# Performance work log

Hardware: AMD Instinct MI355X
Metric: run time of the kernel (lower is better)

Reference implementation:

```python
import jax, jax.numpy as jnp
import numpy as np

B, S, E, H = 8, 512, 1024, 16
Dh = E // H
MAX_LEN = 512


def setup_inputs() -> dict:
    key = jax.random.key(0)
    ks = jax.random.split(key, 16)
    std = 1.0 / np.sqrt(E)
    inp = {
        "query": jax.random.normal(ks[0], (B, S, E), jnp.float32),
        "key": jax.random.normal(ks[1], (B, S, E), jnp.float32),
        "value": jax.random.normal(ks[2], (B, S, E), jnp.float32),
        "Wq": jax.random.normal(ks[3], (E, E), jnp.float32) * std,
        "bq": jax.random.normal(ks[4], (E,), jnp.float32) * std,
        "Wk": jax.random.normal(ks[5], (E, E), jnp.float32) * std,
        "bk": jax.random.normal(ks[6], (E,), jnp.float32) * std,
        "Wv": jax.random.normal(ks[7], (E, E), jnp.float32) * std,
        "bv": jax.random.normal(ks[8], (E,), jnp.float32) * std,
        "Wo": jax.random.normal(ks[9], (E, E), jnp.float32) * std,
        "bo": jax.random.normal(ks[10], (E,), jnp.float32) * std,
        "pos": jax.random.normal(ks[11], (MAX_LEN, 1, E), jnp.float32),
    }
    return inp


def reference(query, key, value, Wq, bq, Wk, bk, Wv, bv, Wo, bo, pos):
    b, sq, e = query.shape
    s = min(sq, key.shape[1])  # target_seq_length (static)
    scale = np.sqrt(Dh).astype(np.float32)
    pe = pos[:s, 0, :][None]  # [1, s, E] broadcast over batch
    q = query[:, :s] @ Wq.T + bq + pe
    k = key[:, :s] @ Wk.T + bk + pe
    v = value[:, :s] @ Wv.T + bv + pe
    # [b, s, H, Dh]
    q = q.reshape(b, s, H, Dh)
    k = k.reshape(b, s, H, Dh)
    v = v.reshape(b, s, H, Dh)
    scores = jnp.einsum("bqhd,bkhd->bhqk", q, k) / scale
    attn = jax.nn.softmax(scores, axis=-1)
    wv = jnp.einsum("bhqk,bkhd->bqhd", attn, v).reshape(b, s, e)
    return wv @ Wo.T + bo
```

## Files before the change

kernel.cpp:

```cpp
#include <hip/hip_runtime.h>
#include <hip/hip_bf16.h>

typedef __attribute__((ext_vector_type(8))) short bfx8;
typedef __attribute__((ext_vector_type(4))) short bfx4;
typedef __attribute__((ext_vector_type(4))) float fx4;

static __device__ __forceinline__ short f2bf(float f) {
  union { float f; unsigned u; } v; v.f = f;
  unsigned r = v.u + 0x7fffu + ((v.u >> 16) & 1u);
  return (short)(r >> 16);
}

static __device__ __forceinline__ void gld16(const void* g, void* l) {
  __builtin_amdgcn_global_load_lds(
      (const __attribute__((address_space(1))) void*)g,
      (__attribute__((address_space(3))) void*)l, 16, 0, 0);
}

constexpr int Bz = 8, Sq = 512, Em = 1024, Hn = 16, Dh = 64;
constexpr int Mrows = Bz * Sq;
constexpr size_t NE = (size_t)Mrows * Em;
constexpr size_t WE = (size_t)Em * Em;

__global__ __launch_bounds__(256) void convert_kernel(
    const float* __restrict__ q, const float* __restrict__ k,
    const float* __restrict__ v,
    const float* __restrict__ Wq, const float* __restrict__ Wk,
    const float* __restrict__ Wv, const float* __restrict__ Wo,
    short* __restrict__ qx, short* __restrict__ kx, short* __restrict__ vx,
    short* __restrict__ wqb, short* __restrict__ wkb,
    short* __restrict__ wvb, short* __restrict__ wob)
{
  const size_t c = (size_t)blockIdx.x * 256 + threadIdx.x;
  constexpr size_t CI = NE / 8;
  constexpr size_t CW = WE / 8;
  const float* src; short* dst; size_t off;
  if (c < 3 * CI) {
    const int sgi = (int)(c / CI);
    src = sgi == 0 ? q : sgi == 1 ? k : v;
    dst = sgi == 0 ? qx : sgi == 1 ? kx : vx;
    off = (c - (size_t)sgi * CI) * 8;
  } else {
    const size_t w = c - 3 * CI;
    const int sgi = (int)(w / CW);
    src = sgi == 0 ? Wq : sgi == 1 ? Wk : sgi == 2 ? Wv : Wo;
    dst = sgi == 0 ? wqb : sgi == 1 ? wkb : sgi == 2 ? wvb : wob;
    off = (w - (size_t)sgi * CW) * 8;
  }
  fx4 a = *(const fx4*)(src + off);
  fx4 b = *(const fx4*)(src + off + 4);
  bfx8 o = { f2bf(a[0]), f2bf(a[1]), f2bf(a[2]), f2bf(a[3]),
             f2bf(b[0]), f2bf(b[1]), f2bf(b[2]), f2bf(b[3]) };
  *(bfx8*)(dst + off) = o;
}

constexpr int LDP = 136;

__global__ __launch_bounds__(256) void gemm_qkv_bf16(
    const short* __restrict__ qx, const short* __restrict__ kx,
    const short* __restrict__ vx,
    const short* __restrict__ Wqb, const short* __restrict__ Wkb,
    const short* __restrict__ Wvb,
    const float* __restrict__ bq, const float* __restrict__ bk,
    const float* __restrict__ bv,
    const float* __restrict__ pos,
    short* __restrict__ qb, short* __restrict__ kb, short* __restrict__ vb)
{
  __shared__ short SM[128 * LDP];
  short* As = SM;
  short* Bs = SM + 4096;

  const int z = blockIdx.z;
  const short* X = (z == 0) ? qx : (z == 1) ? kx : vx;
  const short* W = (z == 0) ? Wqb : (z == 1) ? Wkb : Wvb;
  const float* bias = (z == 0) ? bq : (z == 1) ? bk : bv;
  short* dst = (z == 0) ? qb : (z == 1) ? kb : vb;

  const int m0 = blockIdx.x * 128;
  const int n0 = blockIdx.y * 128;
  const int t = threadIdx.x, lane = t & 63, wave = t >> 6;
  const int wr = wave >> 1, wc = wave & 1;
  const int fr = lane & 15, fq = lane >> 4;

  const int r0 = t >> 2, o0 = (t & 3) * 8;
  const int r1 = r0 + 64;
  short* lA0 = As + wave * 512;
  short* lA1 = As + 2048 + wave * 512;
  short* lB0 = Bs + wave * 512;
  short* lB1 = Bs + 2048 + wave * 512;

  fx4 acc[4][4] = {};

  for (int k0 = 0; k0 < Em; k0 += 32) {
    gld16(W + (size_t)(n0 + r0) * Em + k0 + o0, lA0);
    gld16(W + (size_t)(n0 + r1) * Em + k0 + o0, lA1);
    gld16(X + (size_t)(m0 + r0) * Em + k0 + o0, lB0);
    gld16(X + (size_t)(m0 + r1) * Em + k0 + o0, lB1);
    __syncthreads();

    bfx8 af[4], bf[4];
#pragma unroll
    for (int u = 0; u < 4; ++u)
      af[u] = *(const bfx8*)&As[(wr * 64 + u * 16 + fr) * 32 + fq * 8];
#pragma unroll
    for (int v = 0; v < 4; ++v)
      bf[v] = *(const bfx8*)&Bs[(wc * 64 + v * 16 + fr) * 32 + fq * 8];
#pragma unroll
    for (int u = 0; u < 4; ++u)
#pragma unroll
      for (int v = 0; v < 4; ++v)
        acc[u][v] = __builtin_amdgcn_mfma_f32_16x16x32_bf16(af[u], bf[v], acc[u][v], 0, 0, 0);
    __syncthreads();
  }

  const int rr = t >> 4, jj = t & 15;
  const int b = m0 >> 9;
  if (z < 2) {
#pragma unroll
    for (int u = 0; u < 4; ++u) {
      const int nn = wr * 64 + u * 16 + fq * 4;
      const int nng = n0 + nn;
      const fx4 bb = *(const fx4*)&bias[nng];
#pragma unroll
      for (int v = 0; v < 4; ++v) {
        const int m = wc * 64 + v * 16 + fr;
        const int s = (m0 + m) & (Sq - 1);
        const fx4 pe = *(const fx4*)&pos[(size_t)s * Em + nng];
        const fx4 a = acc[u][v];
        bfx4 o = { f2bf(a[0] + bb[0] + pe[0]), f2bf(a[1] + bb[1] + pe[1]),
                   f2bf(a[2] + bb[2] + pe[2]), f2bf(a[3] + bb[3] + pe[3]) };
        *(bfx4*)&SM[m * LDP + nn] = o;
      }
    }
    __syncthreads();
#pragma unroll
    for (int it = 0; it < 8; ++it) {
      const int m = it * 16 + rr;
      const int s = (m0 + m) & (Sq - 1);
      bfx8 val = *(const bfx8*)&SM[m * LDP + jj * 8];
      const int nng = n0 + jj * 8;
      const int h = nng >> 6, d = nng & 63;
      *(bfx8*)&dst[(((size_t)b * Hn + h) * Sq + s) * Dh + d] = val;
    }
  } else {
#pragma unroll
    for (int u = 0; u < 4; ++u) {
      const int nnb = wr * 64 + u * 16 + fq * 4;
      const int nng = n0 + nnb;
      const fx4 bb = *(const fx4*)&bias[nng];
#pragma unroll
      for (int v = 0; v < 4; ++v) {
        const int m = wc * 64 + v * 16 + fr;
        const int s = (m0 + m) & (Sq - 1);
        const fx4 pe = *(const fx4*)&pos[(size_t)s * Em + nng];
        const fx4 a = acc[u][v];
#pragma unroll
        for (int i = 0; i < 4; ++i) {
          const int row = nnb + i;
          SM[row * LDP + (m ^ ((row & 12) << 2))] = f2bf(a[i] + bb[i] + pe[i]);
        }
      }
    }
    __syncthreads();
    const int s0 = m0 & (Sq - 1);
#pragma unroll
    for (int it = 0; it < 8; ++it) {
      const int row = it * 16 + rr;
      bfx8 val = *(const bfx8*)&SM[row * LDP + ((jj * 8) ^ ((row & 12) << 2))];
      const int nng = n0 + row;
      const int h = nng >> 6, d = nng & 63;
      *(bfx8*)&dst[(((size_t)b * Hn + h) * Dh + d) * Sq + s0 + jj * 8] = val;
    }
  }
}

__global__ __launch_bounds__(256) void gemm_out_bf16(
    const short* __restrict__ wv, const short* __restrict__ Wob,
    const float* __restrict__ bo, float* __restrict__ out)
{
  __shared__ short As[128 * 32];
  __shared__ short Bs[128 * 32];

  const int m0 = blockIdx.x * 128;
  const int n0 = blockIdx.y * 128;
  const int t = threadIdx.x, lane = t & 63, wave = t >> 6;
  const int wr = wave >> 1, wc = wave & 1;
  const int fr = lane & 15, fq = lane >> 4;

  const int r0 = t >> 2, o0 = (t & 3) * 8;
  const int r1 = r0 + 64;
  short* lA0 = As + wave * 512;
  short* lA1 = As + 2048 + wave * 512;
  short* lB0 = Bs + wave * 512;
  short* lB1 = Bs + 2048 + wave * 512;

  fx4 acc[4][4] = {};

  for (int k0 = 0; k0 < Em; k0 += 32) {
    gld16(Wob + (size_t)(n0 + r0) * Em + k0 + o0, lA0);
    gld16(Wob + (size_t)(n0 + r1) * Em + k0 + o0, lA1);
    gld16(wv + (size_t)(m0 + r0) * Em + k0 + o0, lB0);
    gld16(wv + (size_t)(m0 + r1) * Em + k0 + o0, lB1);
    __syncthreads();

    bfx8 af[4], bf[4];
#pragma unroll
    for (int u = 0; u < 4; ++u)
      af[u] = *(const bfx8*)&As[(wr * 64 + u * 16 + fr) * 32 + fq * 8];
#pragma unroll
    for (int v = 0; v < 4; ++v)
      bf[v] = *(const bfx8*)&Bs[(wc * 64 + v * 16 + fr) * 32 + fq * 8];
#pragma unroll
    for (int u = 0; u < 4; ++u)
#pragma unroll
      for (int v = 0; v < 4; ++v)
        acc[u][v] = __builtin_amdgcn_mfma_f32_16x16x32_bf16(af[u], bf[v], acc[u][v], 0, 0, 0);
    __syncthreads();
  }

#pragma unroll
  for (int u = 0; u < 4; ++u) {
    const int nn = n0 + wr * 64 + u * 16 + fq * 4;
    const fx4 bb = *(const fx4*)&bo[nn];
#pragma unroll
    for (int v = 0; v < 4; ++v) {
      const int m = m0 + wc * 64 + v * 16 + fr;
      fx4 val = acc[u][v];
      val[0] += bb[0]; val[1] += bb[1]; val[2] += bb[2]; val[3] += bb[3];
      *(fx4*)&out[(size_t)m * Em + nn] = val;
    }
  }
}

constexpr int KVB = 64, LDK = 72;

__global__ __launch_bounds__(256) void attn_kernel(
    const short* __restrict__ qb, const short* __restrict__ kb,
    const short* __restrict__ vb, short* __restrict__ wv)
{
  __shared__ short Ks[KVB * LDK];
  __shared__ short Vt[Dh * LDK];
  __shared__ short Ps[4][16 * LDK];

  const int bh = blockIdx.x;
  const int qt = blockIdx.y;
  const int t = threadIdx.x, lane = t & 63, wave = t >> 6;
  const int fr = lane & 15, fq = lane >> 4;

  const size_t base = (size_t)bh * Sq * Dh;
  const int q0 = qt * 64 + wave * 16;

  bfx8 qf[2];
  {
    const short* qp = qb + base + (size_t)(q0 + fr) * Dh;
    qf[0] = *(const bfx8*)(qp + fq * 8);
    qf[1] = *(const bfx8*)(qp + 32 + fq * 8);
  }

  float mrow[4] = { -1e30f, -1e30f, -1e30f, -1e30f };
  float lrow[4] = { 0.f, 0.f, 0.f, 0.f };
  fx4 oacc[4] = {};

  const int kr = t >> 2, kc = (t & 3) * 16;

  for (int kv0 = 0; kv0 < Sq; kv0 += KVB) {
    {
      const short* kp = kb + base + (size_t)(kv0 + kr) * Dh + kc;
      bfx8 u0 = *(const bfx8*)kp;
      bfx8 u1 = *(const bfx8*)(kp + 8);
      *(bfx8*)&Ks[kr * LDK + kc] = u0;
      *(bfx8*)&Ks[kr * LDK + kc + 8] = u1;
    }
    {
      const short* vp = vb + base + (size_t)kr * Sq + kv0 + kc;
      bfx8 u0 = *(const bfx8*)vp;
      bfx8 u1 = *(const bfx8*)(vp + 8);
      *(bfx8*)&Vt[kr * LDK + kc] = u0;
      *(bfx8*)&Vt[kr * LDK + kc + 8] = u1;
    }
    __syncthreads();

    fx4 sa[4] = {};
#pragma unroll
    for (int nf = 0; nf < 4; ++nf) {
#pragma unroll
      for (int ks = 0; ks < 2; ++ks) {
        bfx8 kf = *(const bfx8*)&Ks[(nf * 16 + fr) * LDK + ks * 32 + fq * 8];
        sa[nf] = __builtin_amdgcn_mfma_f32_16x16x32_bf16(qf[ks], kf, sa[nf], 0, 0, 0);
      }
    }

#pragma unroll
    for (int i = 0; i < 4; ++i) {
      float mx = fmaxf(fmaxf(sa[0][i], sa[1][i]), fmaxf(sa[2][i], sa[3][i]));
      mx = fmaxf(mx, __shfl_xor(mx, 1));
      mx = fmaxf(mx, __shfl_xor(mx, 2));
      mx = fmaxf(mx, __shfl_xor(mx, 4));
      mx = fmaxf(mx, __shfl_xor(mx, 8));
      mx *= 0.125f;
      const float mn = fmaxf(mrow[i], mx);
      const float alpha = __expf(mrow[i] - mn);
      mrow[i] = mn;
      float rs = 0.f;
#pragma unroll
      for (int nf = 0; nf < 4; ++nf) {
        const float p = __expf(sa[nf][i] * 0.125f - mn);
        rs += p;
        Ps[wave][(fq * 4 + i) * LDK + nf * 16 + fr] = f2bf(p);
      }
      rs += __shfl_xor(rs, 1);
      rs += __shfl_xor(rs, 2);
      rs += __shfl_xor(rs, 4);
      rs += __shfl_xor(rs, 8);
      lrow[i] = lrow[i] * alpha + rs;
#pragma unroll
      for (int df = 0; df < 4; ++df) oacc[df][i] *= alpha;
    }
    __syncthreads();

    bfx8 pf[2];
    pf[0] = *(const bfx8*)&Ps[wave][fr * LDK + fq * 8];
    pf[1] = *(const bfx8*)&Ps[wave][fr * LDK + 32 + fq * 8];
#pragma unroll
    for (int df = 0; df < 4; ++df) {
#pragma unroll
      for (int ks = 0; ks < 2; ++ks) {
        bfx8 vf = *(const bfx8*)&Vt[(df * 16 + fr) * LDK + ks * 32 + fq * 8];
        oacc[df] = __builtin_amdgcn_mfma_f32_16x16x32_bf16(pf[ks], vf, oacc[df], 0, 0, 0);
      }
    }
    __syncthreads();
  }

  const int b = bh >> 4, h = bh & 15;
#pragma unroll
  for (int df = 0; df < 4; ++df) {
    const int d = df * 16 + fr;
#pragma unroll
    for (int i = 0; i < 4; ++i) {
      const int qrow = q0 + fq * 4 + i;
      const float o = oacc[df][i] / lrow[i];
      wv[((size_t)b * Sq + qrow) * Em + h * Dh + d] = f2bf(o);
    }
  }
}

extern "C" void kernel_launch(void* const* d_in, const int* in_sizes, int n_in,
                              void* d_out, int out_size, void* d_ws, size_t ws_size,
                              hipStream_t stream) {
  (void)in_sizes; (void)n_in; (void)out_size; (void)ws_size;
  const float* query = (const float*)d_in[0];
  const float* key   = (const float*)d_in[1];
  const float* value = (const float*)d_in[2];
  const float* Wq = (const float*)d_in[3];
  const float* bq = (const float*)d_in[4];
  const float* Wk = (const float*)d_in[5];
  const float* bk = (const float*)d_in[6];
  const float* Wv = (const float*)d_in[7];
  const float* bv = (const float*)d_in[8];
  const float* Wo = (const float*)d_in[9];
  const float* bo = (const float*)d_in[10];
  const float* pos = (const float*)d_in[11];

  short* qx = (short*)d_ws;
  short* kx = qx + NE;
  short* vx = kx + NE;
  short* Wqb = vx + NE;
  short* Wkb = Wqb + WE;
  short* Wvb = Wkb + WE;
  short* Wob = Wvb + WE;
  short* qb = Wob + WE;
  short* wv = qx;
  short* kb = (short*)d_out;
  short* vb = kb + NE;

  convert_kernel<<<dim3(8192), 256, 0, stream>>>(
      query, key, value, Wq, Wk, Wv, Wo, qx, kx, vx, Wqb, Wkb, Wvb, Wob);
  gemm_qkv_bf16<<<dim3(Mrows / 128, Em / 128, 3), 256, 0, stream>>>(
      qx, kx, vx, Wqb, Wkb, Wvb, bq, bk, bv, pos, qb, kb, vb);
  attn_kernel<<<dim3(Bz * Hn, Sq / 64), 256, 0, stream>>>(qb, kb, vb, wv);
  gemm_out_bf16<<<dim3(Mrows / 128, Em / 128), 256, 0, stream>>>(
      wv, Wob, bo, (float*)d_out);
}
```

Measured before the change: 125.5 us.

## Double-buffer LDS tiles in QKV and output projection GEMMs

```diff
diff --git a/kernel.cpp b/kernel.cpp
--- a/kernel.cpp
+++ b/kernel.cpp
@@ -67,8 +67,6 @@
     short* __restrict__ qb, short* __restrict__ kb, short* __restrict__ vb)
 {
   __shared__ short SM[128 * LDP];
-  short* As = SM;
-  short* Bs = SM + 4096;
 
   const int z = blockIdx.z;
   const short* X = (z == 0) ? qx : (z == 1) ? kx : vx;
@@ -84,32 +82,47 @@
 
   const int r0 = t >> 2, o0 = (t & 3) * 8;
   const int r1 = r0 + 64;
-  short* lA0 = As + wave * 512;
-  short* lA1 = As + 2048 + wave * 512;
-  short* lB0 = Bs + wave * 512;
-  short* lB1 = Bs + 2048 + wave * 512;
+  const short* gW0 = W + (size_t)(n0 + r0) * Em + o0;
+  const short* gW1 = W + (size_t)(n0 + r1) * Em + o0;
+  const short* gX0 = X + (size_t)(m0 + r0) * Em + o0;
+  const short* gX1 = X + (size_t)(m0 + r1) * Em + o0;
 
   fx4 acc[4][4] = {};
 
-  for (int k0 = 0; k0 < Em; k0 += 32) {
-    gld16(W + (size_t)(n0 + r0) * Em + k0 + o0, lA0);
-    gld16(W + (size_t)(n0 + r1) * Em + k0 + o0, lA1);
-    gld16(X + (size_t)(m0 + r0) * Em + k0 + o0, lB0);
-    gld16(X + (size_t)(m0 + r1) * Em + k0 + o0, lB1);
-    __syncthreads();
-
+  auto stage = [&](int kk, short* Ab, short* Bb) {
+    gld16(gW0 + kk, Ab + wave * 512);
+    gld16(gW1 + kk, Ab + 2048 + wave * 512);
+    gld16(gX0 + kk, Bb + wave * 512);
+    gld16(gX1 + kk, Bb + 2048 + wave * 512);
+  };
+  auto compute = [&](const short* Asb, const short* Bsb) {
     bfx8 af[4], bf[4];
 #pragma unroll
     for (int u = 0; u < 4; ++u)
-      af[u] = *(const bfx8*)&As[(wr * 64 + u * 16 + fr) * 32 + fq * 8];
+      af[u] = *(const bfx8*)&Asb[(wr * 64 + u * 16 + fr) * 32 + fq * 8];
 #pragma unroll
     for (int v = 0; v < 4; ++v)
-      bf[v] = *(const bfx8*)&Bs[(wc * 64 + v * 16 + fr) * 32 + fq * 8];
+      bf[v] = *(const bfx8*)&Bsb[(wc * 64 + v * 16 + fr) * 32 + fq * 8];
 #pragma unroll
     for (int u = 0; u < 4; ++u)
 #pragma unroll
       for (int v = 0; v < 4; ++v)
         acc[u][v] = __builtin_amdgcn_mfma_f32_16x16x32_bf16(af[u], bf[v], acc[u][v], 0, 0, 0);
+  };
+
+  short* A0 = SM;
+  short* B0 = SM + 4096;
+  short* A1 = SM + 8192;
+  short* B1 = SM + 12288;
+
+  stage(0, A0, B0);
+  __syncthreads();
+  for (int k0 = 0; k0 < Em; k0 += 64) {
+    stage(k0 + 32, A1, B1);
+    compute(A0, B0);
+    __syncthreads();
+    if (k0 + 64 < Em) stage(k0 + 64, A0, B0);
+    compute(A1, B1);
     __syncthreads();
   }
 
@@ -178,8 +191,7 @@
     const short* __restrict__ wv, const short* __restrict__ Wob,
     const float* __restrict__ bo, float* __restrict__ out)
 {
-  __shared__ short As[128 * 32];
-  __shared__ short Bs[128 * 32];
+  __shared__ short SM[4 * 4096];
 
   const int m0 = blockIdx.x * 128;
   const int n0 = blockIdx.y * 128;
@@ -189,32 +201,47 @@
 
   const int r0 = t >> 2, o0 = (t & 3) * 8;
   const int r1 = r0 + 64;
-  short* lA0 = As + wave * 512;
-  short* lA1 = As + 2048 + wave * 512;
-  short* lB0 = Bs + wave * 512;
-  short* lB1 = Bs + 2048 + wave * 512;
+  const short* gW0 = Wob + (size_t)(n0 + r0) * Em + o0;
+  const short* gW1 = Wob + (size_t)(n0 + r1) * Em + o0;
+  const short* gX0 = wv + (size_t)(m0 + r0) * Em + o0;
+  const short* gX1 = wv + (size_t)(m0 + r1) * Em + o0;
 
   fx4 acc[4][4] = {};
 
-  for (int k0 = 0; k0 < Em; k0 += 32) {
-    gld16(Wob + (size_t)(n0 + r0) * Em + k0 + o0, lA0);
-    gld16(Wob + (size_t)(n0 + r1) * Em + k0 + o0, lA1);
-    gld16(wv + (size_t)(m0 + r0) * Em + k0 + o0, lB0);
-    gld16(wv + (size_t)(m0 + r1) * Em + k0 + o0, lB1);
-    __syncthreads();
-
+  auto stage = [&](int kk, short* Ab, short* Bb) {
+    gld16(gW0 + kk, Ab + wave * 512);
+    gld16(gW1 + kk, Ab + 2048 + wave * 512);
+    gld16(gX0 + kk, Bb + wave * 512);
+    gld16(gX1 + kk, Bb + 2048 + wave * 512);
+  };
+  auto compute = [&](const short* Asb, const short* Bsb) {
     bfx8 af[4], bf[4];
 #pragma unroll
     for (int u = 0; u < 4; ++u)
-      af[u] = *(const bfx8*)&As[(wr * 64 + u * 16 + fr) * 32 + fq * 8];
+      af[u] = *(const bfx8*)&Asb[(wr * 64 + u * 16 + fr) * 32 + fq * 8];
 #pragma unroll
     for (int v = 0; v < 4; ++v)
-      bf[v] = *(const bfx8*)&Bs[(wc * 64 + v * 16 + fr) * 32 + fq * 8];
+      bf[v] = *(const bfx8*)&Bsb[(wc * 64 + v * 16 + fr) * 32 + fq * 8];
 #pragma unroll
     for (int u = 0; u < 4; ++u)
 #pragma unroll
       for (int v = 0; v < 4; ++v)
         acc[u][v] = __builtin_amdgcn_mfma_f32_16x16x32_bf16(af[u], bf[v], acc[u][v], 0, 0, 0);
+  };
+
+  short* A0 = SM;
+  short* B0 = SM + 4096;
+  short* A1 = SM + 8192;
+  short* B1 = SM + 12288;
+
+  stage(0, A0, B0);
+  __syncthreads();
+  for (int k0 = 0; k0 < Em; k0 += 64) {
+    stage(k0 + 32, A1, B1);
+    compute(A0, B0);
+    __syncthreads();
+    if (k0 + 64 < Em) stage(k0 + 64, A0, B0);
+    compute(A1, B1);
     __syncthreads();
   }
 
```

Result: slower. 133.4 us (+6.3%).

## Double GEMM K-tile to 64 with XOR-swizzled LDS layout

Applied to the files above, without the earlier changes.

```diff
diff --git a/kernel.cpp b/kernel.cpp
--- a/kernel.cpp
+++ b/kernel.cpp
@@ -56,7 +56,7 @@
 
 constexpr int LDP = 136;
 
-__global__ __launch_bounds__(256) void gemm_qkv_bf16(
+__global__ __launch_bounds__(256, 4) void gemm_qkv_bf16(
     const short* __restrict__ qx, const short* __restrict__ kx,
     const short* __restrict__ vx,
     const short* __restrict__ Wqb, const short* __restrict__ Wkb,
@@ -68,7 +68,7 @@
 {
   __shared__ short SM[128 * LDP];
   short* As = SM;
-  short* Bs = SM + 4096;
+  short* Bs = SM + 8192;
 
   const int z = blockIdx.z;
   const short* X = (z == 0) ? qx : (z == 1) ? kx : vx;
@@ -82,34 +82,42 @@
   const int wr = wave >> 1, wc = wave & 1;
   const int fr = lane & 15, fq = lane >> 4;
 
-  const int r0 = t >> 2, o0 = (t & 3) * 8;
-  const int r1 = r0 + 64;
-  short* lA0 = As + wave * 512;
-  short* lA1 = As + 2048 + wave * 512;
-  short* lB0 = Bs + wave * 512;
-  short* lB1 = Bs + 2048 + wave * 512;
+  const int trow = t >> 3;
+  const int scol = ((t & 7) ^ (trow & 7)) * 8;
+  const short* gW = W + (size_t)(n0 + trow) * Em + scol;
+  const short* gX = X + (size_t)(m0 + trow) * Em + scol;
+  short* lA = As + wave * 512;
+  short* lB = Bs + wave * 512;
+
+  const int sw0 = ((fq ^ (fr & 7)) * 8);
+  const int sw1 = (((4 + fq) ^ (fr & 7)) * 8);
 
   fx4 acc[4][4] = {};
 
-  for (int k0 = 0; k0 < Em; k0 += 32) {
-    gld16(W + (size_t)(n0 + r0) * Em + k0 + o0, lA0);
-    gld16(W + (size_t)(n0 + r1) * Em + k0 + o0, lA1);
-    gld16(X + (size_t)(m0 + r0) * Em + k0 + o0, lB0);
-    gld16(X + (size_t)(m0 + r1) * Em + k0 + o0, lB1);
-    __syncthreads();
-
-    bfx8 af[4], bf[4];
-#pragma unroll
-    for (int u = 0; u < 4; ++u)
-      af[u] = *(const bfx8*)&As[(wr * 64 + u * 16 + fr) * 32 + fq * 8];
-#pragma unroll
-    for (int v = 0; v < 4; ++v)
-      bf[v] = *(const bfx8*)&Bs[(wc * 64 + v * 16 + fr) * 32 + fq * 8];
-#pragma unroll
-    for (int u = 0; u < 4; ++u)
+  for (int k0 = 0; k0 < Em; k0 += 64) {
+#pragma unroll
+    for (int r = 0; r < 4; ++r) {
+      gld16(gW + (size_t)(32 * r) * Em + k0, lA + r * 2048);
+      gld16(gX + (size_t)(32 * r) * Em + k0, lB + r * 2048);
+    }
+    __syncthreads();
+
+#pragma unroll
+    for (int ks = 0; ks < 2; ++ks) {
+      const int sw = ks ? sw1 : sw0;
+      bfx8 af[4], bf[4];
+#pragma unroll
+      for (int u = 0; u < 4; ++u)
+        af[u] = *(const bfx8*)&As[(wr * 64 + u * 16 + fr) * 64 + sw];
 #pragma unroll
       for (int v = 0; v < 4; ++v)
-        acc[u][v] = __builtin_amdgcn_mfma_f32_16x16x32_bf16(af[u], bf[v], acc[u][v], 0, 0, 0);
+        bf[v] = *(const bfx8*)&Bs[(wc * 64 + v * 16 + fr) * 64 + sw];
+#pragma unroll
+      for (int u = 0; u < 4; ++u)
+#pragma unroll
+        for (int v = 0; v < 4; ++v)
+          acc[u][v] = __builtin_amdgcn_mfma_f32_16x16x32_bf16(af[u], bf[v], acc[u][v], 0, 0, 0);
+    }
     __syncthreads();
   }
 
@@ -174,12 +182,13 @@
   }
 }
 
-__global__ __launch_bounds__(256) void gemm_out_bf16(
+__global__ __launch_bounds__(256, 4) void gemm_out_bf16(
     const short* __restrict__ wv, const short* __restrict__ Wob,
     const float* __restrict__ bo, float* __restrict__ out)
 {
-  __shared__ short As[128 * 32];
-  __shared__ short Bs[128 * 32];
+  __shared__ short SM[2 * 8192];
+  short* As = SM;
+  short* Bs = SM + 8192;
 
   const int m0 = blockIdx.x * 128;
   const int n0 = blockIdx.y * 128;
@@ -187,34 +196,42 @@
   const int wr = wave >> 1, wc = wave & 1;
   const int fr = lane & 15, fq = lane >> 4;
 
-  const int r0 = t >> 2, o0 = (t & 3) * 8;
-  const int r1 = r0 + 64;
-  short* lA0 = As + wave * 512;
-  short* lA1 = As + 2048 + wave * 512;
-  short* lB0 = Bs + wave * 512;
-  short* lB1 = Bs + 2048 + wave * 512;
+  const int trow = t >> 3;
+  const int scol = ((t & 7) ^ (trow & 7)) * 8;
+  const short* gW = Wob + (size_t)(n0 + trow) * Em + scol;
+  const short* gX = wv + (size_t)(m0 + trow) * Em + scol;
+  short* lA = As + wave * 512;
+  short* lB = Bs + wave * 512;
+
+  const int sw0 = ((fq ^ (fr & 7)) * 8);
+  const int sw1 = (((4 + fq) ^ (fr & 7)) * 8);
 
   fx4 acc[4][4] = {};
 
-  for (int k0 = 0; k0 < Em; k0 += 32) {
-    gld16(Wob + (size_t)(n0 + r0) * Em + k0 + o0, lA0);
-    gld16(Wob + (size_t)(n0 + r1) * Em + k0 + o0, lA1);
-    gld16(wv + (size_t)(m0 + r0) * Em + k0 + o0, lB0);
-    gld16(wv + (size_t)(m0 + r1) * Em + k0 + o0, lB1);
-    __syncthreads();
-
-    bfx8 af[4], bf[4];
-#pragma unroll
-    for (int u = 0; u < 4; ++u)
-      af[u] = *(const bfx8*)&As[(wr * 64 + u * 16 + fr) * 32 + fq * 8];
-#pragma unroll
-    for (int v = 0; v < 4; ++v)
-      bf[v] = *(const bfx8*)&Bs[(wc * 64 + v * 16 + fr) * 32 + fq * 8];
-#pragma unroll
-    for (int u = 0; u < 4; ++u)
+  for (int k0 = 0; k0 < Em; k0 += 64) {
+#pragma unroll
+    for (int r = 0; r < 4; ++r) {
+      gld16(gW + (size_t)(32 * r) * Em + k0, lA + r * 2048);
+      gld16(gX + (size_t)(32 * r) * Em + k0, lB + r * 2048);
+    }
+    __syncthreads();
+
+#pragma unroll
+    for (int ks = 0; ks < 2; ++ks) {
+      const int sw = ks ? sw1 : sw0;
+      bfx8 af[4], bf[4];
+#pragma unroll
+      for (int u = 0; u < 4; ++u)
+        af[u] = *(const bfx8*)&As[(wr * 64 + u * 16 + fr) * 64 + sw];
 #pragma unroll
       for (int v = 0; v < 4; ++v)
-        acc[u][v] = __builtin_amdgcn_mfma_f32_16x16x32_bf16(af[u], bf[v], acc[u][v], 0, 0, 0);
+        bf[v] = *(const bfx8*)&Bs[(wc * 64 + v * 16 + fr) * 64 + sw];
+#pragma unroll
+      for (int u = 0; u < 4; ++u)
+#pragma unroll
+        for (int v = 0; v < 4; ++v)
+          acc[u][v] = __builtin_amdgcn_mfma_f32_16x16x32_bf16(af[u], bf[v], acc[u][v], 0, 0, 0);
+    }
     __syncthreads();
   }
 
```

Result: faster. 116.4 us (-7.2%).
